# Kernel optimization log

Hardware: AMD Instinct MI355X
Metric: run time of the kernel (lower is better)

The kernel has to match this reference:

```python
import jax, jax.numpy as jnp
import numpy as np

SIZE = (4096, 4096)   # self.size
SIGMA = 1.0           # blur_sigma
NOISE_STD = 0.01      # noise_std


def _gauss_kernel(sigma):
    # scipy.ndimage.gaussian_filter: radius = int(truncate*sigma + 0.5), truncate=4.0
    r = int(4.0 * sigma + 0.5)
    x = np.arange(-r, r + 1, dtype=np.float32)
    k = np.exp(-0.5 * (x / sigma) ** 2)
    k = k / k.sum()
    return jnp.asarray(k), r


def _blur(img, sigma):
    # img: [C, H, W]; separable Gaussian, scipy mode='reflect' == jnp symmetric pad
    k, r = _gauss_kernel(sigma)
    x = jnp.pad(img, ((0, 0), (r, r), (r, r)), mode='symmetric')
    x = x[:, None]  # [C, 1, H+2r, W+2r] (NCHW)
    kh = k.reshape(1, 1, -1, 1)
    kw = k.reshape(1, 1, 1, -1)
    x = jax.lax.conv_general_dilated(x, kh, (1, 1), 'VALID')
    x = jax.lax.conv_general_dilated(x, kw, (1, 1), 'VALID')
    return x[:, 0]  # [C, H, W]


def setup_inputs() -> dict:
    key = jax.random.key(0)
    k1, k2 = jax.random.split(key)
    img = jax.random.normal(k1, (1, 2048, 2048), dtype=jnp.float32)
    noise = jax.random.normal(k2, (1,) + SIZE, dtype=jnp.float32)
    return {"img": img, "noise": noise}


def reference(img, noise):
    # bilinear resize, align_corners=False == jax half-pixel linear resize
    img = jax.image.resize(img, (img.shape[0],) + SIZE, method='linear')
    img = jnp.flip(img, axis=2)   # horizontal flip
    img = jnp.flip(img, axis=1)   # vertical flip
    img = jnp.rot90(img, k=1, axes=(1, 2))  # rot90, k fixed to 1
    img = img + noise * NOISE_STD
    img = _blur(img, SIGMA)
    img = jnp.log1p(jnp.clip(img, 0.0))  # clamp(min=0) then log1p
    return img
```

## Files before the change

### kernel.cpp

```cpp
#include <hip/hip_runtime.h>
#include <math.h>

#define N      4096
#define NIMG   2048
#define SPAN   128
#define TXN    120
#define HRW    16
#define PP     66
#define PR     66
#define NSX    35
#define NSY    64
#define NBLK   (NSX * NSY)

#define KW0 0.00013383063f
#define KW1 0.00443186160f
#define KW2 0.05399112800f
#define KW3 0.24197144000f
#define KW4 0.39894346870f

__device__ __forceinline__ int symi(int g) {
    g = (g < 0) ? (-1 - g) : g;
    g = (g >= N) ? (2 * N - 1 - g) : g;
    return g;
}

#define H9(A,B,C,D,E,F,G,H,I)                                                  \
    fmaf(KW0,(A), fmaf(KW1,(B), fmaf(KW2,(C), fmaf(KW3,(D), fmaf(KW4,(E),      \
    fmaf(KW3,(F), fmaf(KW2,(G), fmaf(KW1,(H), KW0*(I)))))))))

#define GCOL2(J, G) do {                                                       \
    const float p0_ = ipg[(J) - PP];                                           \
    const float p1_ = ipg[(J)];                                                \
    const float p2_ = ipg[(J) + PP];                                           \
    (G).x = fmaf(0.75f, p1_, 0.25f * p2_);                                     \
    (G).y = fmaf(0.25f, p0_, 0.75f * p1_);                                     \
} while (0)

#define PROD4(J2, D0, D1, D2, D3, Z0, Z1, Z2, Z3) do {                         \
    float2 gc_, gd_;                                                           \
    GCOL2((J2), gc_); GCOL2((J2) + 1, gd_);                                    \
    (D0).x = fmaf(0.25f, ga.x, fmaf(0.75f, gb.x, 0.01f * (Z0).x));             \
    (D0).y = fmaf(0.25f, ga.y, fmaf(0.75f, gb.y, 0.01f * (Z0).y));             \
    (D1).x = fmaf(0.75f, gb.x, fmaf(0.25f, gc_.x, 0.01f * (Z1).x));            \
    (D1).y = fmaf(0.75f, gb.y, fmaf(0.25f, gc_.y, 0.01f * (Z1).y));            \
    (D2).x = fmaf(0.25f, gb.x, fmaf(0.75f, gc_.x, 0.01f * (Z2).x));            \
    (D2).y = fmaf(0.25f, gb.y, fmaf(0.75f, gc_.y, 0.01f * (Z2).y));            \
    (D3).x = fmaf(0.75f, gc_.x, fmaf(0.25f, gd_.x, 0.01f * (Z3).x));           \
    (D3).y = fmaf(0.75f, gc_.y, fmaf(0.25f, gd_.y, 0.01f * (Z3).y));           \
    ga = gc_; gb = gd_;                                                        \
} while (0)

#define OUT1(K, GY) do {                                                       \
    float2 v_;                                                                 \
    v_.x = H9(win[K].x, win[K+1].x, win[K+2].x, win[K+3].x, win[K+4].x,        \
              win[K+5].x, win[K+6].x, win[K+7].x, win[K+8].x);                 \
    v_.y = H9(win[K].y, win[K+1].y, win[K+2].y, win[K+3].y, win[K+4].y,        \
              win[K+5].y, win[K+6].y, win[K+7].y, win[K+8].y);                 \
    float* sl_ = ((K) & 1) ? EX1 : EX0;                                        \
    *reinterpret_cast<float2*>(sl_ + 2 * lane) = v_;                           \
    const float2 l0_ = *reinterpret_cast<const float2*>(sl_ + oL0);            \
    const float2 l1_ = *reinterpret_cast<const float2*>(sl_ + oL1);            \
    const float2 r0_ = *reinterpret_cast<const float2*>(sl_ + oR0);            \
    const float2 r1_ = *reinterpret_cast<const float2*>(sl_ + oR1);            \
    float ox_ = KW0 * l0_.x; ox_ = fmaf(KW1, l0_.y, ox_);                      \
    ox_ = fmaf(KW2, l1_.x, ox_); ox_ = fmaf(KW3, l1_.y, ox_);                  \
    ox_ = fmaf(KW4, v_.x, ox_);  ox_ = fmaf(KW3, v_.y, ox_);                   \
    ox_ = fmaf(KW2, r0_.x, ox_); ox_ = fmaf(KW1, r0_.y, ox_);                  \
    ox_ = fmaf(KW0, r1_.x, ox_);                                               \
    float oy_ = KW0 * l0_.y; oy_ = fmaf(KW1, l1_.x, oy_);                      \
    oy_ = fmaf(KW2, l1_.y, oy_); oy_ = fmaf(KW3, v_.x, oy_);                   \
    oy_ = fmaf(KW4, v_.y, oy_);  oy_ = fmaf(KW3, r0_.x, oy_);                  \
    oy_ = fmaf(KW2, r0_.y, oy_); oy_ = fmaf(KW1, r1_.x, oy_);                  \
    oy_ = fmaf(KW0, r1_.y, oy_);                                               \
    float2 rr_;                                                                \
    rr_.x = __logf(1.0f + fmaxf(ox_, 0.0f));                                   \
    rr_.y = __logf(1.0f + fmaxf(oy_, 0.0f));                                   \
    if (okst) *reinterpret_cast<float2*>(out + (size_t)(GY) * N + gxs) = rr_;  \
} while (0)

#define SLIDE4() do {                                                          \
    _Pragma("unroll")                                                          \
    for (int i_ = 0; i_ < 8; ++i_) win[i_] = win[i_ + 4];                      \
} while (0)

__global__ __launch_bounds__(256, 5)
void TensorAugment_79216376807666_kernel(const float* __restrict__ img,
                                         const float* __restrict__ noise,
                                         float* __restrict__ out) {
    __shared__ __align__(16) float SH[PR * PP + 4 * 256];

    const int tid  = threadIdx.x;
    const int lane = tid & 63;
    const int wave = tid >> 6;

    float* const IP  = SH;
    float* const EX0 = SH + PR * PP + wave * 256;
    float* const EX1 = EX0 + 128;

    const int bid = blockIdx.x;
    const int sx  = bid % NSX;
    const int sy  = bid / NSX;
    const int x0  = sx * TXN;
    const int y0  = sy * 64;

    int gxa = x0 - 4, gxb = x0 + SPAN - 5;
    int mxa = symi(gxa), mxb = symi(gxb);
    int gxmin = min(mxa, mxb), gxmax = max(mxa, mxb);
    if (gxa <= 0) gxmin = 0;
    if (gxb >= N - 1) gxmax = N - 1;
    int umin = (N - 1) - gxmax, umax = (N - 1) - gxmin;
    int r0min = (umin - 1) >> 1;
    int r0max = (umax - 1) >> 1;
    int nrows = r0max - r0min + 2;

    int gya = y0 - 4, gyb = y0 + 67;
    int mya = symi(gya), myb = symi(gyb);
    int gymin = min(mya, myb), gymax = max(mya, myb);
    if (gya <= 0) gymin = 0;
    if (gyb >= N - 1) gymax = N - 1;
    int c0min = (gymin - 1) >> 1;

    {
        const int gcol = min(max(c0min + lane, 0), NIMG - 1);
        for (int r = wave; r < nrows; r += 4) {
            const int ir = min(max(r0min + r, 0), NIMG - 1);
            IP[r * PP + lane] = img[ir * NIMG + gcol];
        }
    }
    __syncthreads();

    const int y0w = y0 + HRW * wave;
    const int gxs = x0 - 4 + 2 * lane;
    const bool okst = (lane >= 2) && (lane <= 61) && (gxs <= N - 2);
    const bool yin  = (y0w >= 4) && (y0w + 19 <= N - 1);
    const bool xin  = (sx > 0) && (sx < NSX - 1);
    const int oL0 = max(2 * lane - 4, 0), oL1 = max(2 * lane - 2, 0);
    const int oR0 = min(2 * lane + 2, 126), oR1 = min(2 * lane + 4, 126);

    float2 win[12];

    if (xin && yin) {
        const int a    = (x0 >> 1) - 2 + lane;
        const int ipb  = (2047 - a - r0min) * PP;
        const float* const ipg = IP + ipb;
        const int jb   = ((y0w - 5) >> 1) - c0min;
        const float* const nzb = noise + ((size_t)(y0w - 4) * N + gxs);
#define LDNZ(DR) (*reinterpret_cast<const float2*>(nzb + (size_t)(DR) * N))

        float2 ga, gb;
        GCOL2(jb, ga);
        GCOL2(jb + 1, gb);

        {
            float2 n0 = LDNZ(0), n1 = LDNZ(1), n2 = LDNZ(2),  n3 = LDNZ(3);
            float2 n4 = LDNZ(4), n5 = LDNZ(5), n6 = LDNZ(6),  n7 = LDNZ(7);
            float2 n8 = LDNZ(8), n9 = LDNZ(9), na = LDNZ(10), nb = LDNZ(11);
            PROD4(jb + 2, win[0], win[1], win[2],  win[3],  n0, n1, n2, n3);
            PROD4(jb + 4, win[4], win[5], win[6],  win[7],  n4, n5, n6, n7);
            PROD4(jb + 6, win[8], win[9], win[10], win[11], n8, n9, na, nb);
        }
        {
            float2 n0 = LDNZ(12), n1 = LDNZ(13), n2 = LDNZ(14), n3 = LDNZ(15);
            OUT1(0, y0w + 0); OUT1(1, y0w + 1); OUT1(2, y0w + 2); OUT1(3, y0w + 3);
            SLIDE4();
            PROD4(jb + 8, win[8], win[9], win[10], win[11], n0, n1, n2, n3);
        }
        {
            float2 n0 = LDNZ(16), n1 = LDNZ(17), n2 = LDNZ(18), n3 = LDNZ(19);
            OUT1(0, y0w + 4); OUT1(1, y0w + 5); OUT1(2, y0w + 6); OUT1(3, y0w + 7);
            SLIDE4();
            PROD4(jb + 10, win[8], win[9], win[10], win[11], n0, n1, n2, n3);
        }
        {
            float2 n0 = LDNZ(20), n1 = LDNZ(21), n2 = LDNZ(22), n3 = LDNZ(23);
            OUT1(0, y0w + 8); OUT1(1, y0w + 9); OUT1(2, y0w + 10); OUT1(3, y0w + 11);
            SLIDE4();
            PROD4(jb + 12, win[8], win[9], win[10], win[11], n0, n1, n2, n3);
        }
        OUT1(0, y0w + 12); OUT1(1, y0w + 13); OUT1(2, y0w + 14); OUT1(3, y0w + 15);
#undef LDNZ
    } else {
        const int gxm0 = symi(gxs), gxm1 = symi(gxs + 1);
        const int u0 = (N - 1) - gxm0, u1 = (N - 1) - gxm1;
        const int A0 = (((u0 - 1) >> 1) - r0min) * PP;
        const int A1 = (((u1 - 1) >> 1) - r0min) * PP;
        const float w10 = (u0 & 1) ? 0.25f : 0.75f, w00 = 1.0f - w10;
        const float w11 = (u1 & 1) ? 0.25f : 0.75f, w01 = 1.0f - w11;

        auto nzg = [&](int dr) -> float2 {
            const float* nr = noise + (size_t)symi(y0w - 4 + dr) * N;
            float2 r; r.x = nr[gxm0]; r.y = nr[gxm1]; return r;
        };
        auto dgen = [&](int dr, float2 nz) -> float2 {
            const int gym = symi(y0w - 4 + dr);
            const int jc  = ((gym - 1) >> 1) - c0min;
            const float wc1 = (gym & 1) ? 0.25f : 0.75f;
            const float wc0 = 1.0f - wc1;
            float2 r;
            {
                const float t = fmaf(wc0, IP[A0 + jc], wc1 * IP[A0 + jc + 1]);
                const float b = fmaf(wc0, IP[A0 + PP + jc], wc1 * IP[A0 + PP + jc + 1]);
                r.x = fmaf(w00, t, fmaf(w10, b, 0.01f * nz.x));
            }
            {
                const float t = fmaf(wc0, IP[A1 + jc], wc1 * IP[A1 + jc + 1]);
                const float b = fmaf(wc0, IP[A1 + PP + jc], wc1 * IP[A1 + PP + jc + 1]);
                r.y = fmaf(w01, t, fmaf(w11, b, 0.01f * nz.y));
            }
            return r;
        };

#pragma unroll
        for (int j = 0; j < 12; ++j) win[j] = dgen(j, nzg(j));

#pragma unroll
        for (int c = 0; c < 4; ++c) {
            float2 n0, n1, n2, n3;
            if (c < 3) { n0 = nzg(12 + 4 * c); n1 = nzg(13 + 4 * c);
                         n2 = nzg(14 + 4 * c); n3 = nzg(15 + 4 * c); }
            OUT1(0, y0w + 4 * c + 0); OUT1(1, y0w + 4 * c + 1);
            OUT1(2, y0w + 4 * c + 2); OUT1(3, y0w + 4 * c + 3);
            if (c < 3) {
                SLIDE4();
                win[8]  = dgen(12 + 4 * c, n0);
                win[9]  = dgen(13 + 4 * c, n1);
                win[10] = dgen(14 + 4 * c, n2);
                win[11] = dgen(15 + 4 * c, n3);
            }
        }
    }
}

extern "C" void kernel_launch(void* const* d_in, const int* in_sizes, int n_in,
                              void* d_out, int out_size, void* d_ws, size_t ws_size,
                              hipStream_t stream) {
    const float* img   = (const float*)d_in[0];
    const float* noise = (const float*)d_in[1];
    float* out = (float*)d_out;

    dim3 grid(NBLK);
    TensorAugment_79216376807666_kernel<<<grid, 256, 0, stream>>>(img, noise, out);
}
```

Before: 140.6 us.

## Load image tile via direct global-to-LDS and prefetch noise before barrier

The image tile is now staged with global_load_lds, which writes straight into shared memory without going through registers, using a fixed 17-row unrolled loop. The padded row count grows to 68 so the fixed loop stays in bounds. The first 12 noise rows are loaded into registers before the barrier so their latency overlaps the LDS fill. Edge tiles are remapped to the lowest block indices so the slow boundary path starts first, and the occupancy hint rises from 5 to 6 waves per SIMD. The trade-offs are some redundant row loads, a larger LDS footprint, and more register pressure from the prefetched noise.

```diff
diff --git a/kernel.cpp b/kernel.cpp
--- a/kernel.cpp
+++ b/kernel.cpp
@@ -7,7 +7,8 @@
 #define TXN    120
 #define HRW    16
 #define PP     66
-#define PR     66
+#define PR     68
+#define IPOFF  (PR * PP)
 #define NSX    35
 #define NSY    64
 #define NBLK   (NSX * NSY)
@@ -22,6 +23,12 @@
     g = (g < 0) ? (-1 - g) : g;
     g = (g >= N) ? (2 * N - 1 - g) : g;
     return g;
+}
+
+__device__ __forceinline__ void gload_lds4(const float* g, float* l) {
+    __builtin_amdgcn_global_load_lds(
+        (const __attribute__((address_space(1))) unsigned int*)g,
+        (__attribute__((address_space(3))) unsigned int*)l, 4, 0, 0);
 }
 
 #define H9(A,B,C,D,E,F,G,H,I)                                                  \
@@ -83,25 +90,26 @@
     for (int i_ = 0; i_ < 8; ++i_) win[i_] = win[i_ + 4];                      \
 } while (0)
 
-__global__ __launch_bounds__(256, 5)
+__global__ __launch_bounds__(256, 6)
 void TensorAugment_79216376807666_kernel(const float* __restrict__ img,
                                          const float* __restrict__ noise,
                                          float* __restrict__ out) {
-    __shared__ __align__(16) float SH[PR * PP + 4 * 256];
+    __shared__ __align__(16) float SH[IPOFF + 4 * 256];
 
     const int tid  = threadIdx.x;
     const int lane = tid & 63;
     const int wave = tid >> 6;
 
     float* const IP  = SH;
-    float* const EX0 = SH + PR * PP + wave * 256;
+    float* const EX0 = SH + IPOFF + wave * 256;
     float* const EX1 = EX0 + 128;
 
     const int bid = blockIdx.x;
-    const int sx  = bid % NSX;
-    const int sy  = bid / NSX;
-    const int x0  = sx * TXN;
-    const int y0  = sy * 64;
+    int sx, sy;
+    if (bid < 2 * NSY) { sy = bid >> 1; sx = (bid & 1) ? (NSX - 1) : 0; }
+    else { const int t = bid - 2 * NSY; sx = 1 + t % (NSX - 2); sy = t / (NSX - 2); }
+    const int x0 = sx * TXN;
+    const int y0 = sy * 64;
 
     int gxa = x0 - 4, gxb = x0 + SPAN - 5;
     int mxa = symi(gxa), mxb = symi(gxb);
@@ -119,46 +127,53 @@
     if (gya <= 0) gymin = 0;
     if (gyb >= N - 1) gymax = N - 1;
     int c0min = (gymin - 1) >> 1;
+    (void)nrows;
 
     {
         const int gcol = min(max(c0min + lane, 0), NIMG - 1);
-        for (int r = wave; r < nrows; r += 4) {
+#pragma unroll
+        for (int k = 0; k < 17; ++k) {
+            const int r  = wave + 4 * k;
             const int ir = min(max(r0min + r, 0), NIMG - 1);
-            IP[r * PP + lane] = img[ir * NIMG + gcol];
+            gload_lds4(img + (size_t)ir * NIMG + gcol, IP + r * PP);
         }
     }
-    __syncthreads();
 
     const int y0w = y0 + HRW * wave;
     const int gxs = x0 - 4 + 2 * lane;
     const bool okst = (lane >= 2) && (lane <= 61) && (gxs <= N - 2);
     const bool yin  = (y0w >= 4) && (y0w + 19 <= N - 1);
     const bool xin  = (sx > 0) && (sx < NSX - 1);
+    const bool fast = xin && yin;
     const int oL0 = max(2 * lane - 4, 0), oL1 = max(2 * lane - 2, 0);
     const int oR0 = min(2 * lane + 2, 126), oR1 = min(2 * lane + 4, 126);
 
+    const int a    = (x0 >> 1) - 2 + lane;
+    const int ipb  = (2047 - a - r0min) * PP;
+    const float* const ipg = IP + ipb;
+    const int jb   = ((y0w - 5) >> 1) - c0min;
+    const float* const nzb = noise + ((size_t)(y0w - 4) * N + gxs);
+#define LDNZ(DR) (*reinterpret_cast<const float2*>(nzb + (size_t)(DR) * N))
+
+    float2 npre[12];
+    if (fast) {
+#pragma unroll
+        for (int j = 0; j < 12; ++j) npre[j] = LDNZ(j);
+    }
+
+    __syncthreads();
+
     float2 win[12];
 
-    if (xin && yin) {
-        const int a    = (x0 >> 1) - 2 + lane;
-        const int ipb  = (2047 - a - r0min) * PP;
-        const float* const ipg = IP + ipb;
-        const int jb   = ((y0w - 5) >> 1) - c0min;
-        const float* const nzb = noise + ((size_t)(y0w - 4) * N + gxs);
-#define LDNZ(DR) (*reinterpret_cast<const float2*>(nzb + (size_t)(DR) * N))
-
+    if (fast) {
         float2 ga, gb;
         GCOL2(jb, ga);
         GCOL2(jb + 1, gb);
 
-        {
-            float2 n0 = LDNZ(0), n1 = LDNZ(1), n2 = LDNZ(2),  n3 = LDNZ(3);
-            float2 n4 = LDNZ(4), n5 = LDNZ(5), n6 = LDNZ(6),  n7 = LDNZ(7);
-            float2 n8 = LDNZ(8), n9 = LDNZ(9), na = LDNZ(10), nb = LDNZ(11);
-            PROD4(jb + 2, win[0], win[1], win[2],  win[3],  n0, n1, n2, n3);
-            PROD4(jb + 4, win[4], win[5], win[6],  win[7],  n4, n5, n6, n7);
-            PROD4(jb + 6, win[8], win[9], win[10], win[11], n8, n9, na, nb);
-        }
+        PROD4(jb + 2, win[0], win[1], win[2],  win[3],  npre[0], npre[1], npre[2],  npre[3]);
+        PROD4(jb + 4, win[4], win[5], win[6],  win[7],  npre[4], npre[5], npre[6],  npre[7]);
+        PROD4(jb + 6, win[8], win[9], win[10], win[11], npre[8], npre[9], npre[10], npre[11]);
+
         {
             float2 n0 = LDNZ(12), n1 = LDNZ(13), n2 = LDNZ(14), n3 = LDNZ(15);
             OUT1(0, y0w + 0); OUT1(1, y0w + 1); OUT1(2, y0w + 2); OUT1(3, y0w + 3);
@@ -178,7 +193,6 @@
             PROD4(jb + 12, win[8], win[9], win[10], win[11], n0, n1, n2, n3);
         }
         OUT1(0, y0w + 12); OUT1(1, y0w + 13); OUT1(2, y0w + 14); OUT1(3, y0w + 15);
-#undef LDNZ
     } else {
         const int gxm0 = symi(gxs), gxm1 = symi(gxs + 1);
         const int u0 = (N - 1) - gxm0, u1 = (N - 1) - gxm1;
@@ -229,6 +243,7 @@
             }
         }
     }
+#undef LDNZ
 }
 
 extern "C" void kernel_launch(void* const* d_in, const int* in_sizes, int n_in,
```

Measured after the change: 144.0 us. 1.02x slower.

## Widen tiles to four columns per lane and prefetch noise before barrier

Applied to the files above, without the earlier changes.

Each lane now produces four output columns (float4) instead of two, and tiles are widened from 120 to 248 columns, so halo overhead and block count shrink. The horizontal blur now needs only neighbour-lane float4 exchanges through LDS instead of four float2 reads. The first twelve noise rows are loaded before the shared-memory barrier to overlap global latency with the image tile staging. The trade-off is more registers per thread (float4 windows), which may lower occupancy under the 256x5 launch bound, and fewer blocks for the GPU.

```diff
diff --git a/kernel.cpp b/kernel.cpp
--- a/kernel.cpp
+++ b/kernel.cpp
@@ -3,12 +3,13 @@
 
 #define N      4096
 #define NIMG   2048
-#define SPAN   128
-#define TXN    120
+#define TXN    248
+#define BSPAN  260
 #define HRW    16
-#define PP     66
-#define PR     66
-#define NSX    35
+#define PPI    39
+#define PR     132
+#define IPSZ   (PR * PPI)
+#define NSX    17
 #define NSY    64
 #define NBLK   (NSX * NSY)
 
@@ -28,54 +29,58 @@
     fmaf(KW0,(A), fmaf(KW1,(B), fmaf(KW2,(C), fmaf(KW3,(D), fmaf(KW4,(E),      \
     fmaf(KW3,(F), fmaf(KW2,(G), fmaf(KW1,(H), KW0*(I)))))))))
 
-#define GCOL2(J, G) do {                                                       \
-    const float p0_ = ipg[(J) - PP];                                           \
+#define GCOL4(J, G) do {                                                       \
+    const float pm_ = ipg[(J) - 2 * PPI];                                      \
+    const float p0_ = ipg[(J) - PPI];                                          \
     const float p1_ = ipg[(J)];                                                \
-    const float p2_ = ipg[(J) + PP];                                           \
+    const float p2_ = ipg[(J) + PPI];                                          \
     (G).x = fmaf(0.75f, p1_, 0.25f * p2_);                                     \
     (G).y = fmaf(0.25f, p0_, 0.75f * p1_);                                     \
+    (G).z = fmaf(0.75f, p0_, 0.25f * p1_);                                     \
+    (G).w = fmaf(0.25f, pm_, 0.75f * p0_);                                     \
+} while (0)
+
+#define DM4(DST, W0, GA_, W1, GB_, NZ) do {                                    \
+    (DST).x = fmaf(W0, (GA_).x, fmaf(W1, (GB_).x, 0.01f * (NZ).x));            \
+    (DST).y = fmaf(W0, (GA_).y, fmaf(W1, (GB_).y, 0.01f * (NZ).y));            \
+    (DST).z = fmaf(W0, (GA_).z, fmaf(W1, (GB_).z, 0.01f * (NZ).z));            \
+    (DST).w = fmaf(W0, (GA_).w, fmaf(W1, (GB_).w, 0.01f * (NZ).w));            \
 } while (0)
 
 #define PROD4(J2, D0, D1, D2, D3, Z0, Z1, Z2, Z3) do {                         \
-    float2 gc_, gd_;                                                           \
-    GCOL2((J2), gc_); GCOL2((J2) + 1, gd_);                                    \
-    (D0).x = fmaf(0.25f, ga.x, fmaf(0.75f, gb.x, 0.01f * (Z0).x));             \
-    (D0).y = fmaf(0.25f, ga.y, fmaf(0.75f, gb.y, 0.01f * (Z0).y));             \
-    (D1).x = fmaf(0.75f, gb.x, fmaf(0.25f, gc_.x, 0.01f * (Z1).x));            \
-    (D1).y = fmaf(0.75f, gb.y, fmaf(0.25f, gc_.y, 0.01f * (Z1).y));            \
-    (D2).x = fmaf(0.25f, gb.x, fmaf(0.75f, gc_.x, 0.01f * (Z2).x));            \
-    (D2).y = fmaf(0.25f, gb.y, fmaf(0.75f, gc_.y, 0.01f * (Z2).y));            \
-    (D3).x = fmaf(0.75f, gc_.x, fmaf(0.25f, gd_.x, 0.01f * (Z3).x));           \
-    (D3).y = fmaf(0.75f, gc_.y, fmaf(0.25f, gd_.y, 0.01f * (Z3).y));           \
+    float4 gc_, gd_;                                                           \
+    GCOL4((J2), gc_); GCOL4((J2) + 1, gd_);                                    \
+    DM4(D0, 0.25f, ga,  0.75f, gb,  Z0);                                       \
+    DM4(D1, 0.75f, gb,  0.25f, gc_, Z1);                                       \
+    DM4(D2, 0.25f, gb,  0.75f, gc_, Z2);                                       \
+    DM4(D3, 0.75f, gc_, 0.25f, gd_, Z3);                                       \
     ga = gc_; gb = gd_;                                                        \
 } while (0)
 
 #define OUT1(K, GY) do {                                                       \
-    float2 v_;                                                                 \
+    float4 v_;                                                                 \
     v_.x = H9(win[K].x, win[K+1].x, win[K+2].x, win[K+3].x, win[K+4].x,        \
               win[K+5].x, win[K+6].x, win[K+7].x, win[K+8].x);                 \
     v_.y = H9(win[K].y, win[K+1].y, win[K+2].y, win[K+3].y, win[K+4].y,        \
               win[K+5].y, win[K+6].y, win[K+7].y, win[K+8].y);                 \
+    v_.z = H9(win[K].z, win[K+1].z, win[K+2].z, win[K+3].z, win[K+4].z,        \
+              win[K+5].z, win[K+6].z, win[K+7].z, win[K+8].z);                 \
+    v_.w = H9(win[K].w, win[K+1].w, win[K+2].w, win[K+3].w, win[K+4].w,        \
+              win[K+5].w, win[K+6].w, win[K+7].w, win[K+8].w);                 \
     float* sl_ = ((K) & 1) ? EX1 : EX0;                                        \
-    *reinterpret_cast<float2*>(sl_ + 2 * lane) = v_;                           \
-    const float2 l0_ = *reinterpret_cast<const float2*>(sl_ + oL0);            \
-    const float2 l1_ = *reinterpret_cast<const float2*>(sl_ + oL1);            \
-    const float2 r0_ = *reinterpret_cast<const float2*>(sl_ + oR0);            \
-    const float2 r1_ = *reinterpret_cast<const float2*>(sl_ + oR1);            \
-    float ox_ = KW0 * l0_.x; ox_ = fmaf(KW1, l0_.y, ox_);                      \
-    ox_ = fmaf(KW2, l1_.x, ox_); ox_ = fmaf(KW3, l1_.y, ox_);                  \
-    ox_ = fmaf(KW4, v_.x, ox_);  ox_ = fmaf(KW3, v_.y, ox_);                   \
-    ox_ = fmaf(KW2, r0_.x, ox_); ox_ = fmaf(KW1, r0_.y, ox_);                  \
-    ox_ = fmaf(KW0, r1_.x, ox_);                                               \
-    float oy_ = KW0 * l0_.y; oy_ = fmaf(KW1, l1_.x, oy_);                      \
-    oy_ = fmaf(KW2, l1_.y, oy_); oy_ = fmaf(KW3, v_.x, oy_);                   \
-    oy_ = fmaf(KW4, v_.y, oy_);  oy_ = fmaf(KW3, r0_.x, oy_);                  \
-    oy_ = fmaf(KW2, r0_.y, oy_); oy_ = fmaf(KW1, r1_.x, oy_);                  \
-    oy_ = fmaf(KW0, r1_.y, oy_);                                               \
-    float2 rr_;                                                                \
-    rr_.x = __logf(1.0f + fmaxf(ox_, 0.0f));                                   \
-    rr_.y = __logf(1.0f + fmaxf(oy_, 0.0f));                                   \
-    if (okst) *reinterpret_cast<float2*>(out + (size_t)(GY) * N + gxs) = rr_;  \
+    *reinterpret_cast<float4*>(sl_ + 4 * lane) = v_;                           \
+    const float4 wl_ = *reinterpret_cast<const float4*>(sl_ + 4 * lnL);        \
+    const float4 wr_ = *reinterpret_cast<const float4*>(sl_ + 4 * lnR);        \
+    float4 rr_;                                                                \
+    rr_.x = H9(wl_.x, wl_.y, wl_.z, wl_.w, v_.x, v_.y, v_.z, v_.w, wr_.x);     \
+    rr_.y = H9(wl_.y, wl_.z, wl_.w, v_.x, v_.y, v_.z, v_.w, wr_.x, wr_.y);     \
+    rr_.z = H9(wl_.z, wl_.w, v_.x, v_.y, v_.z, v_.w, wr_.x, wr_.y, wr_.z);     \
+    rr_.w = H9(wl_.w, v_.x, v_.y, v_.z, v_.w, wr_.x, wr_.y, wr_.z, wr_.w);     \
+    rr_.x = __logf(1.0f + fmaxf(rr_.x, 0.0f));                                 \
+    rr_.y = __logf(1.0f + fmaxf(rr_.y, 0.0f));                                 \
+    rr_.z = __logf(1.0f + fmaxf(rr_.z, 0.0f));                                 \
+    rr_.w = __logf(1.0f + fmaxf(rr_.w, 0.0f));                                 \
+    if (okst) *reinterpret_cast<float4*>(out + (size_t)(GY) * N + gxs) = rr_;  \
 } while (0)
 
 #define SLIDE4() do {                                                          \
@@ -87,15 +92,15 @@
 void TensorAugment_79216376807666_kernel(const float* __restrict__ img,
                                          const float* __restrict__ noise,
                                          float* __restrict__ out) {
-    __shared__ __align__(16) float SH[PR * PP + 4 * 256];
+    __shared__ __align__(16) float SH[IPSZ + 4 * 512];
 
     const int tid  = threadIdx.x;
     const int lane = tid & 63;
     const int wave = tid >> 6;
 
     float* const IP  = SH;
-    float* const EX0 = SH + PR * PP + wave * 256;
-    float* const EX1 = EX0 + 128;
+    float* const EX0 = SH + IPSZ + wave * 512;
+    float* const EX1 = EX0 + 256;
 
     const int bid = blockIdx.x;
     const int sx  = bid % NSX;
@@ -103,7 +108,7 @@
     const int x0  = sx * TXN;
     const int y0  = sy * 64;
 
-    int gxa = x0 - 4, gxb = x0 + SPAN - 5;
+    int gxa = x0 - 4, gxb = x0 + BSPAN - 5;
     int mxa = symi(gxa), mxb = symi(gxb);
     int gxmin = min(mxa, mxb), gxmax = max(mxa, mxb);
     if (gxa <= 0) gxmin = 0;
@@ -120,92 +125,119 @@
     if (gyb >= N - 1) gymax = N - 1;
     int c0min = (gymin - 1) >> 1;
 
+    int ncols = ((gymax - 1) >> 1) - c0min + 2;
+
     {
-        const int gcol = min(max(c0min + lane, 0), NIMG - 1);
-        for (int r = wave; r < nrows; r += 4) {
-            const int ir = min(max(r0min + r, 0), NIMG - 1);
-            IP[r * PP + lane] = img[ir * NIMG + gcol];
+        const int c = lane;
+        if (c < ncols) {
+            const int ic = min(max(c0min + c, 0), NIMG - 1);
+            for (int r = wave; r < nrows; r += 4) {
+                const int ir = min(max(r0min + r, 0), NIMG - 1);
+                IP[r * PPI + c] = img[(size_t)ir * NIMG + ic];
+            }
         }
     }
+
+    const int y0w = y0 + HRW * wave;
+    const int gxs = x0 - 4 + 4 * lane;
+    const bool okst = (lane >= 1) && (lane <= 62) && (gxs >= 0) && (gxs <= N - 4);
+    const bool xin  = (sx > 0) && (sx < NSX - 1);
+    const bool yin  = (y0w >= 4) && (y0w + 19 <= N - 1);
+    const bool fast = xin && yin;
+    const int lnL = (lane == 0) ? 0 : lane - 1;
+    const int lnR = (lane == 63) ? 63 : lane + 1;
+
+    const int a    = gxs >> 1;
+    const int ipb  = (2047 - a - r0min) * PPI;
+    const float* const ipg = IP + ipb;
+    const int jb   = ((y0w - 5) >> 1) - c0min;
+    const float* const nzb = noise + ((size_t)(y0w - 4) * N + gxs);
+#define LDNZ(DR) (*reinterpret_cast<const float4*>(nzb + (size_t)(DR) * N))
+
+    float4 np0, np1, np2, np3, np4, np5, np6, np7, np8, np9, npa, npb;
+    if (fast) {
+        np0 = LDNZ(0);  np1 = LDNZ(1);  np2 = LDNZ(2);  np3 = LDNZ(3);
+        np4 = LDNZ(4);  np5 = LDNZ(5);  np6 = LDNZ(6);  np7 = LDNZ(7);
+        np8 = LDNZ(8);  np9 = LDNZ(9);  npa = LDNZ(10); npb = LDNZ(11);
+    }
+
     __syncthreads();
 
-    const int y0w = y0 + HRW * wave;
-    const int gxs = x0 - 4 + 2 * lane;
-    const bool okst = (lane >= 2) && (lane <= 61) && (gxs <= N - 2);
-    const bool yin  = (y0w >= 4) && (y0w + 19 <= N - 1);
-    const bool xin  = (sx > 0) && (sx < NSX - 1);
-    const int oL0 = max(2 * lane - 4, 0), oL1 = max(2 * lane - 2, 0);
-    const int oR0 = min(2 * lane + 2, 126), oR1 = min(2 * lane + 4, 126);
-
-    float2 win[12];
-
-    if (xin && yin) {
-        const int a    = (x0 >> 1) - 2 + lane;
-        const int ipb  = (2047 - a - r0min) * PP;
-        const float* const ipg = IP + ipb;
-        const int jb   = ((y0w - 5) >> 1) - c0min;
-        const float* const nzb = noise + ((size_t)(y0w - 4) * N + gxs);
-#define LDNZ(DR) (*reinterpret_cast<const float2*>(nzb + (size_t)(DR) * N))
-
-        float2 ga, gb;
-        GCOL2(jb, ga);
-        GCOL2(jb + 1, gb);
+    float4 win[12];
+
+    if (fast) {
+        float4 ga, gb;
+        GCOL4(jb, ga);
+        GCOL4(jb + 1, gb);
+
+        PROD4(jb + 2, win[0], win[1], win[2],  win[3],  np0, np1, np2, np3);
+        PROD4(jb + 4, win[4], win[5], win[6],  win[7],  np4, np5, np6, np7);
+        PROD4(jb + 6, win[8], win[9], win[10], win[11], np8, np9, npa, npb);
 
         {
-            float2 n0 = LDNZ(0), n1 = LDNZ(1), n2 = LDNZ(2),  n3 = LDNZ(3);
-            float2 n4 = LDNZ(4), n5 = LDNZ(5), n6 = LDNZ(6),  n7 = LDNZ(7);
-            float2 n8 = LDNZ(8), n9 = LDNZ(9), na = LDNZ(10), nb = LDNZ(11);
-            PROD4(jb + 2, win[0], win[1], win[2],  win[3],  n0, n1, n2, n3);
-            PROD4(jb + 4, win[4], win[5], win[6],  win[7],  n4, n5, n6, n7);
-            PROD4(jb + 6, win[8], win[9], win[10], win[11], n8, n9, na, nb);
-        }
-        {
-            float2 n0 = LDNZ(12), n1 = LDNZ(13), n2 = LDNZ(14), n3 = LDNZ(15);
+            float4 n0 = LDNZ(12), n1 = LDNZ(13), n2 = LDNZ(14), n3 = LDNZ(15);
             OUT1(0, y0w + 0); OUT1(1, y0w + 1); OUT1(2, y0w + 2); OUT1(3, y0w + 3);
             SLIDE4();
             PROD4(jb + 8, win[8], win[9], win[10], win[11], n0, n1, n2, n3);
         }
         {
-            float2 n0 = LDNZ(16), n1 = LDNZ(17), n2 = LDNZ(18), n3 = LDNZ(19);
+            float4 n0 = LDNZ(16), n1 = LDNZ(17), n2 = LDNZ(18), n3 = LDNZ(19);
             OUT1(0, y0w + 4); OUT1(1, y0w + 5); OUT1(2, y0w + 6); OUT1(3, y0w + 7);
             SLIDE4();
             PROD4(jb + 10, win[8], win[9], win[10], win[11], n0, n1, n2, n3);
         }
         {
-            float2 n0 = LDNZ(20), n1 = LDNZ(21), n2 = LDNZ(22), n3 = LDNZ(23);
+            float4 n0 = LDNZ(20), n1 = LDNZ(21), n2 = LDNZ(22), n3 = LDNZ(23);
             OUT1(0, y0w + 8); OUT1(1, y0w + 9); OUT1(2, y0w + 10); OUT1(3, y0w + 11);
             SLIDE4();
             PROD4(jb + 12, win[8], win[9], win[10], win[11], n0, n1, n2, n3);
         }
         OUT1(0, y0w + 12); OUT1(1, y0w + 13); OUT1(2, y0w + 14); OUT1(3, y0w + 15);
-#undef LDNZ
     } else {
-        const int gxm0 = symi(gxs), gxm1 = symi(gxs + 1);
+        const int gxm0 = symi(gxs + 0), gxm1 = symi(gxs + 1);
+        const int gxm2 = symi(gxs + 2), gxm3 = symi(gxs + 3);
         const int u0 = (N - 1) - gxm0, u1 = (N - 1) - gxm1;
-        const int A0 = (((u0 - 1) >> 1) - r0min) * PP;
-        const int A1 = (((u1 - 1) >> 1) - r0min) * PP;
+        const int u2 = (N - 1) - gxm2, u3 = (N - 1) - gxm3;
+        const int A0 = (((u0 - 1) >> 1) - r0min) * PPI;
+        const int A1 = (((u1 - 1) >> 1) - r0min) * PPI;
+        const int A2 = (((u2 - 1) >> 1) - r0min) * PPI;
+        const int A3 = (((u3 - 1) >> 1) - r0min) * PPI;
         const float w10 = (u0 & 1) ? 0.25f : 0.75f, w00 = 1.0f - w10;
         const float w11 = (u1 & 1) ? 0.25f : 0.75f, w01 = 1.0f - w11;
-
-        auto nzg = [&](int dr) -> float2 {
+        const float w12 = (u2 & 1) ? 0.25f : 0.75f, w02 = 1.0f - w12;
+        const float w13 = (u3 & 1) ? 0.25f : 0.75f, w03 = 1.0f - w13;
+
+        auto nzg = [&](int dr) -> float4 {
             const float* nr = noise + (size_t)symi(y0w - 4 + dr) * N;
-            float2 r; r.x = nr[gxm0]; r.y = nr[gxm1]; return r;
+            float4 r;
+            r.x = nr[gxm0]; r.y = nr[gxm1]; r.z = nr[gxm2]; r.w = nr[gxm3];
+            return r;
         };
-        auto dgen = [&](int dr, float2 nz) -> float2 {
+        auto dgen = [&](int dr, float4 nz) -> float4 {
             const int gym = symi(y0w - 4 + dr);
             const int jc  = ((gym - 1) >> 1) - c0min;
             const float wc1 = (gym & 1) ? 0.25f : 0.75f;
             const float wc0 = 1.0f - wc1;
-            float2 r;
+            float4 r;
             {
                 const float t = fmaf(wc0, IP[A0 + jc], wc1 * IP[A0 + jc + 1]);
-                const float b = fmaf(wc0, IP[A0 + PP + jc], wc1 * IP[A0 + PP + jc + 1]);
+                const float b = fmaf(wc0, IP[A0 + PPI + jc], wc1 * IP[A0 + PPI + jc + 1]);
                 r.x = fmaf(w00, t, fmaf(w10, b, 0.01f * nz.x));
             }
             {
                 const float t = fmaf(wc0, IP[A1 + jc], wc1 * IP[A1 + jc + 1]);
-                const float b = fmaf(wc0, IP[A1 + PP + jc], wc1 * IP[A1 + PP + jc + 1]);
+                const float b = fmaf(wc0, IP[A1 + PPI + jc], wc1 * IP[A1 + PPI + jc + 1]);
                 r.y = fmaf(w01, t, fmaf(w11, b, 0.01f * nz.y));
+            }
+            {
+                const float t = fmaf(wc0, IP[A2 + jc], wc1 * IP[A2 + jc + 1]);
+                const float b = fmaf(wc0, IP[A2 + PPI + jc], wc1 * IP[A2 + PPI + jc + 1]);
+                r.z = fmaf(w02, t, fmaf(w12, b, 0.01f * nz.z));
+            }
+            {
+                const float t = fmaf(wc0, IP[A3 + jc], wc1 * IP[A3 + jc + 1]);
+                const float b = fmaf(wc0, IP[A3 + PPI + jc], wc1 * IP[A3 + PPI + jc + 1]);
+                r.w = fmaf(w03, t, fmaf(w13, b, 0.01f * nz.w));
             }
             return r;
         };
@@ -215,7 +247,7 @@
 
 #pragma unroll
         for (int c = 0; c < 4; ++c) {
-            float2 n0, n1, n2, n3;
+            float4 n0, n1, n2, n3;
             if (c < 3) { n0 = nzg(12 + 4 * c); n1 = nzg(13 + 4 * c);
                          n2 = nzg(14 + 4 * c); n3 = nzg(15 + 4 * c); }
             OUT1(0, y0w + 4 * c + 0); OUT1(1, y0w + 4 * c + 1);
@@ -229,6 +261,7 @@
             }
         }
     }
+#undef LDNZ
 }
 
 extern "C" void kernel_launch(void* const* d_in, const int* in_sizes, int n_in,
```

Result: slower. 188.8 us (+34.3%).
